# Kernel tuning notes

Hardware: AMD Instinct MI355X
Metric: run time of the kernel (lower is better)

## Reference

```python
import jax, jax.numpy as jnp
import numpy as np

ALPHA = 0.1  # config['alpha']


def setup_inputs() -> dict:
    key = jax.random.key(0)
    k1, k2, k3, k4, k5 = jax.random.split(key, 5)
    n_bs, bit, n_cls, class_bit, n_train = 128, 48, 100, 16, 10000
    u = jax.random.normal(k1, (n_bs, bit), dtype=jnp.float32)
    # multi-hot labels (float, as in torch: y.float())
    y = jax.random.bernoulli(k2, 0.1, (n_bs, n_cls)).astype(jnp.float32)
    ind = jnp.arange(n_bs, dtype=jnp.int64)  # distinct in-range row indices
    # buffers mid-training: U holds previous class-wise codes, Y previous labels
    U = jax.random.normal(k3, (n_train, n_cls, class_bit), dtype=jnp.float32) * 0.1
    Y = jax.random.bernoulli(k4, 0.1, (n_train, n_cls)).astype(jnp.float32)
    # xavier_uniform-like init for w_D [n_class, bit, class_bit]
    limit = np.sqrt(6.0 / (bit + class_bit)).astype(np.float32)
    w_D = jax.random.uniform(k5, (n_cls, bit, class_bit), dtype=jnp.float32,
                             minval=-limit, maxval=limit)
    return {"u": u, "y": y, "ind": ind, "U": U, "Y": Y, "w_D": w_D}


def reference(u, y, ind, U, Y, w_D):
    # update label buffer: self.Y[ind, :] = y
    Y = Y.at[ind].set(y)
    # u_ = matmul(u, w_D).permute(1,0,2): [n_bs, n_cls, class_bit]
    u_ = jnp.einsum('bk,ckd->bcd', u, w_D)
    # update code buffer with detached u_ (torch: self.U[ind] = u_.data)
    U = U.at[ind].set(jax.lax.stop_gradient(u_))
    # pairwise similarity s: [n_bs, n_train, n_cls]
    s = y[:, None, :] * Y[None, :, :]
    # inner_product: sum over class_bit -> [n_bs, n_train, n_cls]
    ip = jnp.einsum('tcd,bcd->btc', U, u_)
    # stable log(1 + exp(ip)) - s*ip, exactly as the torch expression
    likelihood = (jnp.log1p(jnp.exp(-jnp.abs(ip))) + jnp.maximum(ip, 0.0)
                  - s * ip).mean()
    quantization = ALPHA * jnp.mean((u_ - jnp.sign(u_)) ** 2)
    return likelihood + quantization
```

## Files before the change

### kernel.cpp

```cpp
#include <hip/hip_runtime.h>
#include <math.h>

#define CB 16
#define ALPHA 0.1f
#define LOG2E 1.4426950408889634f

typedef __bf16 bf16x8 __attribute__((ext_vector_type(8)));
typedef float  f32x16 __attribute__((ext_vector_type(16)));

__device__ __forceinline__ unsigned int f2bf(float x) {
    unsigned int u = __float_as_uint(x);
    return (u + 0x7FFFu + ((u >> 16) & 1u)) >> 16;
}

__device__ inline float block_reduce_256(float v, float* red) {
    #pragma unroll
    for (int off = 32; off > 0; off >>= 1) v += __shfl_down(v, off, 64);
    int lane = threadIdx.x & 63;
    int wid  = threadIdx.x >> 6;
    if (lane == 0) red[wid] = v;
    __syncthreads();
    float s = 0.f;
    if (threadIdx.x == 0) {
        int nw = blockDim.x >> 6;
        for (int w = 0; w < nw; ++w) s += red[w];
    }
    return s;
}

__global__ __launch_bounds__(256) void compute_u_kernel(
        const float* __restrict__ u, const float* __restrict__ w_D,
        float* __restrict__ u_f32, unsigned short* __restrict__ u_bf,
        float* __restrict__ quant_partials, int* __restrict__ inv,
        int n_bs, int bit, int n_cls, int n_train) {
    __shared__ float red[4];
    int idx = blockIdx.x * blockDim.x + threadIdx.x;
    if (idx < n_train) inv[idx] = -1;
    int total = n_bs * n_cls * CB;
    float q = 0.f;
    if (idx < total) {
        int d = idx & (CB - 1);
        int c = (idx / CB) % n_cls;
        int b = idx / (CB * n_cls);
        const float* __restrict__ ur = u + (size_t)b * bit;
        const float* __restrict__ w  = w_D + (size_t)c * bit * CB + d;
        float s = 0.f;
        for (int k = 0; k < bit; ++k) s = fmaf(ur[k], w[k * CB], s);
        u_f32[idx] = s;
        u_bf[((size_t)c * n_bs + b) * CB + d] = (unsigned short)f2bf(s * LOG2E);
        float sgn = (s > 0.f) ? 1.f : ((s < 0.f) ? -1.f : 0.f);
        float dd = s - sgn;
        q = dd * dd;
    }
    float bs = block_reduce_256(q, red);
    if (threadIdx.x == 0) quant_partials[blockIdx.x] = bs;
}

__global__ __launch_bounds__(256) void compute_vw_kernel(
        const float* __restrict__ y, const float* __restrict__ u_f32,
        const int* __restrict__ ind, int* __restrict__ inv,
        float* __restrict__ vvec, float* __restrict__ wvec,
        int n_bs, int n_cls) {
    if (blockIdx.x == 0 && threadIdx.x < n_bs)
        inv[ind[threadIdx.x]] = threadIdx.x;
    __shared__ float vs[16][17];
    __shared__ float wsh[16][17];
    const int c  = blockIdx.x;
    const int d  = threadIdx.x & (CB - 1);
    const int sl = threadIdx.x >> 4;
    float v = 0.f, w = 0.f;
    const int bpp = n_bs >> 4;
    for (int b = sl * bpp; b < (sl + 1) * bpp; ++b) {
        float x = u_f32[((size_t)b * n_cls + c) * CB + d];
        w += x;
        v = fmaf(y[(size_t)b * n_cls + c], x, v);
    }
    vs[sl][d] = v; wsh[sl][d] = w;
    __syncthreads();
    #pragma unroll
    for (int s = 8; s > 0; s >>= 1) {
        if (sl < s) {
            vs[sl][d]  += vs[sl + s][d];
            wsh[sl][d] += wsh[sl + s][d];
        }
        __syncthreads();
    }
    if (sl == 0) {
        vvec[(size_t)c * CB + d] = vs[0][d];
        wvec[(size_t)c * CB + d] = wsh[0][d];
    }
}

__global__ __launch_bounds__(256) void loss_main_mfma(
        const float* __restrict__ y, const float* __restrict__ U,
        const float* __restrict__ Yb, const float* __restrict__ u_f32,
        const unsigned short* __restrict__ u_bf,
        const float* __restrict__ vvec, const float* __restrict__ wvec,
        const int* __restrict__ inv, float* __restrict__ partials, int nblk,
        int n_bs, int n_cls, int n_train) {
    __shared__ float red[4 * 4];
    const int lane = threadIdx.x & 63;
    const int wid  = threadIdx.x >> 6;
    const int c    = blockIdx.x * 4 + wid;
    const int t0   = blockIdx.y * 32;
    const int r    = lane & 31;
    const int h    = lane >> 5;
    const int row  = t0 + r;

    const bool valid = (row < n_train);
    const int rc = valid ? row : (n_train - 1);
    const int iv = inv[rc];

    const float* __restrict__ arow = (iv >= 0)
        ? (u_f32 + ((size_t)iv * n_cls + c) * CB)
        : (U     + ((size_t)rc * n_cls + c) * CB);
    float4 a0 = *(const float4*)(arow + h * 8);
    float4 a1 = *(const float4*)(arow + h * 8 + 4);
    const float* __restrict__ yrow = (iv >= 0)
        ? (y  + (size_t)iv * n_cls + c)
        : (Yb + (size_t)rc * n_cls + c);
    float Yv = *yrow;
    if (!valid) {
        a0 = make_float4(0.f, 0.f, 0.f, 0.f);
        a1 = make_float4(0.f, 0.f, 0.f, 0.f);
        Yv = 0.f;
    }

    const float* __restrict__ vp = vvec + (size_t)c * CB + h * 8;
    const float* __restrict__ wp = wvec + (size_t)c * CB + h * 8;
    float sv = a0.x*vp[0] + a0.y*vp[1] + a0.z*vp[2] + a0.w*vp[3]
             + a1.x*vp[4] + a1.y*vp[5] + a1.z*vp[6] + a1.w*vp[7];
    float sw = a0.x*wp[0] + a0.y*wp[1] + a0.z*wp[2] + a0.w*wp[3]
             + a1.x*wp[4] + a1.y*wp[5] + a1.z*wp[6] + a1.w*wp[7];
    float sideS = Yv * sv;
    float sideW = sw;

    union { unsigned int u32[4]; bf16x8 v; } A;
    A.u32[0] = f2bf(a0.x) | (f2bf(a0.y) << 16);
    A.u32[1] = f2bf(a0.z) | (f2bf(a0.w) << 16);
    A.u32[2] = f2bf(a1.x) | (f2bf(a1.y) << 16);
    A.u32[3] = f2bf(a1.z) | (f2bf(a1.w) << 16);

    const unsigned short* __restrict__ ub = u_bf + (size_t)c * n_bs * CB;
    bf16x8 B[4];
    #pragma unroll
    for (int bt = 0; bt < 4; ++bt)
        B[bt] = *(const bf16x8*)(ub + (size_t)(bt * 32 + r) * CB + h * 8);

    float accL = 0.f;
    float accA = 0.f;
    f32x16 zc = {};
    #pragma unroll
    for (int bt = 0; bt < 4; ++bt) {
        f32x16 D = __builtin_amdgcn_mfma_f32_32x32x16_bf16(A.v, B[bt], zc, 0, 0, 0);
        float a[16];
        #pragma unroll
        for (int j = 0; j < 16; ++j) {
            float ipa = fabsf(D[j]);
            a[j] = 1.0f + __builtin_amdgcn_exp2f(-ipa);
            accA += ipa;
        }
        #pragma unroll
        for (int s = 1; s < 16; s <<= 1)
            #pragma unroll
            for (int j = 0; j < 16; j += 2 * s) a[j] *= a[j + s];
        accL += __builtin_amdgcn_logf(a[0]);
    }

    #pragma unroll
    for (int off = 32; off > 0; off >>= 1) {
        accL  += __shfl_down(accL,  off, 64);
        accA  += __shfl_down(accA,  off, 64);
        sideS += __shfl_down(sideS, off, 64);
        sideW += __shfl_down(sideW, off, 64);
    }
    if (lane == 0) {
        red[wid * 4 + 0] = accL;
        red[wid * 4 + 1] = accA;
        red[wid * 4 + 2] = sideS;
        red[wid * 4 + 3] = sideW;
    }
    __syncthreads();
    if (threadIdx.x < 4) {
        float s = red[0 * 4 + threadIdx.x] + red[1 * 4 + threadIdx.x]
                + red[2 * 4 + threadIdx.x] + red[3 * 4 + threadIdx.x];
        int bid = blockIdx.y * gridDim.x + blockIdx.x;
        partials[(size_t)threadIdx.x * nblk + bid] = s;
    }
}

__global__ __launch_bounds__(256) void finalize_kernel(
        const float* __restrict__ partials, int nblk,
        const float* __restrict__ quant_partials, int n_quant,
        float* __restrict__ out, double n_pad,
        double like_scale, double quant_scale) {
    double sL = 0, sA = 0, sS = 0, sW = 0, sQ = 0;
    for (int i = threadIdx.x; i < nblk; i += 256) {
        sL += (double)partials[0 * nblk + i];
        sA += (double)partials[1 * nblk + i];
        sS += (double)partials[2 * nblk + i];
        sW += (double)partials[3 * nblk + i];
    }
    for (int i = threadIdx.x; i < n_quant; i += 256) sQ += (double)quant_partials[i];
    #pragma unroll
    for (int off = 32; off > 0; off >>= 1) {
        sL += __shfl_down(sL, off, 64);
        sA += __shfl_down(sA, off, 64);
        sS += __shfl_down(sS, off, 64);
        sW += __shfl_down(sW, off, 64);
        sQ += __shfl_down(sQ, off, 64);
    }
    __shared__ double red[4][5];
    int lane = threadIdx.x & 63, wid = threadIdx.x >> 6;
    if (lane == 0) {
        red[wid][0] = sL; red[wid][1] = sA; red[wid][2] = sS;
        red[wid][3] = sW; red[wid][4] = sQ;
    }
    __syncthreads();
    if (threadIdx.x == 0) {
        double L = 0, Aa = 0, S = 0, W = 0, Q = 0;
        for (int w = 0; w < 4; ++w) {
            L += red[w][0]; Aa += red[w][1]; S += red[w][2];
            W += red[w][3]; Q  += red[w][4];
        }
        const double ln2 = 0.6931471805599453;
        double like = ln2 * (L - n_pad + 0.5 * Aa) + 0.5 * W - S;
        out[0] = (float)(like * like_scale + Q * quant_scale);
    }
}

extern "C" void kernel_launch(void* const* d_in, const int* in_sizes, int n_in,
                              void* d_out, int out_size, void* d_ws, size_t ws_size,
                              hipStream_t stream) {
    const float* u   = (const float*)d_in[0];
    const float* y   = (const float*)d_in[1];
    const int*   ind = (const int*)d_in[2];
    const float* U   = (const float*)d_in[3];
    const float* Yb  = (const float*)d_in[4];
    const float* w_D = (const float*)d_in[5];

    const int n_bs    = in_sizes[2];
    const int bit     = in_sizes[0] / n_bs;
    const int n_cls   = in_sizes[1] / n_bs;
    const int n_train = in_sizes[4] / n_cls;

    const int totalU = n_bs * n_cls * CB;
    const int nub    = (totalU + 255) / 256;
    const int ntile  = (n_train + 31) / 32;
    const int gx     = (n_cls + 3) / 4;
    const int nblk   = ntile * gx;

    char* ws = (char*)d_ws;
    size_t off = 0;
    float* u_f32 = (float*)(ws + off);          off += (size_t)totalU * 4;
    unsigned short* u_bf = (unsigned short*)(ws + off); off += (size_t)totalU * 2;
    off = (off + 15) & ~(size_t)15;
    int* inv = (int*)(ws + off);                off += (size_t)n_train * 4;
    off = (off + 15) & ~(size_t)15;
    float* vvec = (float*)(ws + off);           off += (size_t)n_cls * CB * 4;
    float* wvec = (float*)(ws + off);           off += (size_t)n_cls * CB * 4;
    float* quant_partials = (float*)(ws + off); off += (size_t)nub * 4;
    off = (off + 15) & ~(size_t)15;
    float* partials = (float*)(ws + off);       off += (size_t)nblk * 4 * 4;

    compute_u_kernel<<<nub, 256, 0, stream>>>(u, w_D, u_f32, u_bf,
                                              quant_partials, inv,
                                              n_bs, bit, n_cls, n_train);
    compute_vw_kernel<<<n_cls, 256, 0, stream>>>(y, u_f32, ind, inv,
                                                 vvec, wvec, n_bs, n_cls);
    loss_main_mfma<<<dim3(gx, ntile), 256, 0, stream>>>(
        y, U, Yb, u_f32, u_bf, vvec, wvec, inv, partials, nblk,
        n_bs, n_cls, n_train);

    const double n_pad = (double)((long long)(ntile * 32 - n_train) *
                                  (long long)n_bs * (long long)n_cls);
    const double like_scale  = 1.0 / ((double)n_bs * n_train * n_cls);
    const double quant_scale = (double)ALPHA / (double)totalU;
    finalize_kernel<<<1, 256, 0, stream>>>(partials, nblk, quant_partials, nub,
                                           (float*)d_out, n_pad,
                                           like_scale, quant_scale);
}
```

Measured before the change: 59.79 us.

## Merge prep kernels, drop inverse-index buffer, process two row tiles per wave

Merges the u_ computation and the v/w vector computation into one prep kernel. The v/w vectors are now computed algebraically from sums over u and the weights, so they no longer depend on u_f32 and that pass can run concurrently. The inv scatter buffer is removed; each loss block builds a per-block list of overridden rows from ind in shared memory. Each wave now covers 64 training rows with two A fragments and eight MFMAs, halving the grid and reusing the B loads. This saves one kernel launch and the dependent-launch serialization, at the cost of a per-block scan of ind and a serial patch loop.

```diff
diff --git a/kernel.cpp b/kernel.cpp
--- a/kernel.cpp
+++ b/kernel.cpp
@@ -7,11 +7,6 @@
 
 typedef __bf16 bf16x8 __attribute__((ext_vector_type(8)));
 typedef float  f32x16 __attribute__((ext_vector_type(16)));
-
-__device__ __forceinline__ unsigned int f2bf(float x) {
-    unsigned int u = __float_as_uint(x);
-    return (u + 0x7FFFu + ((u >> 16) & 1u)) >> 16;
-}
 
 __device__ inline float block_reduce_256(float v, float* red) {
     #pragma unroll
@@ -28,120 +23,161 @@
     return s;
 }
 
-__global__ __launch_bounds__(256) void compute_u_kernel(
-        const float* __restrict__ u, const float* __restrict__ w_D,
-        float* __restrict__ u_f32, unsigned short* __restrict__ u_bf,
-        float* __restrict__ quant_partials, int* __restrict__ inv,
-        int n_bs, int bit, int n_cls, int n_train) {
+__global__ __launch_bounds__(256) void prep_kernel(
+        const float* __restrict__ u, const float* __restrict__ y,
+        const float* __restrict__ w_D,
+        float* __restrict__ u_f32, __bf16* __restrict__ u_bf,
+        float* __restrict__ quant_partials,
+        float* __restrict__ vvec, float* __restrict__ wvec,
+        int n_bs, int bit, int n_cls, int nub) {
     __shared__ float red[4];
-    int idx = blockIdx.x * blockDim.x + threadIdx.x;
-    if (idx < n_train) inv[idx] = -1;
-    int total = n_bs * n_cls * CB;
-    float q = 0.f;
-    if (idx < total) {
-        int d = idx & (CB - 1);
-        int c = (idx / CB) % n_cls;
-        int b = idx / (CB * n_cls);
-        const float* __restrict__ ur = u + (size_t)b * bit;
-        const float* __restrict__ w  = w_D + (size_t)c * bit * CB + d;
-        float s = 0.f;
-        for (int k = 0; k < bit; ++k) s = fmaf(ur[k], w[k * CB], s);
-        u_f32[idx] = s;
-        u_bf[((size_t)c * n_bs + b) * CB + d] = (unsigned short)f2bf(s * LOG2E);
-        float sgn = (s > 0.f) ? 1.f : ((s < 0.f) ? -1.f : 0.f);
-        float dd = s - sgn;
-        q = dd * dd;
-    }
-    float bs = block_reduce_256(q, red);
-    if (threadIdx.x == 0) quant_partials[blockIdx.x] = bs;
-}
-
-__global__ __launch_bounds__(256) void compute_vw_kernel(
-        const float* __restrict__ y, const float* __restrict__ u_f32,
-        const int* __restrict__ ind, int* __restrict__ inv,
-        float* __restrict__ vvec, float* __restrict__ wvec,
-        int n_bs, int n_cls) {
-    if (blockIdx.x == 0 && threadIdx.x < n_bs)
-        inv[ind[threadIdx.x]] = threadIdx.x;
-    __shared__ float vs[16][17];
-    __shared__ float wsh[16][17];
-    const int c  = blockIdx.x;
-    const int d  = threadIdx.x & (CB - 1);
-    const int sl = threadIdx.x >> 4;
-    float v = 0.f, w = 0.f;
-    const int bpp = n_bs >> 4;
-    for (int b = sl * bpp; b < (sl + 1) * bpp; ++b) {
-        float x = u_f32[((size_t)b * n_cls + c) * CB + d];
-        w += x;
-        v = fmaf(y[(size_t)b * n_cls + c], x, v);
-    }
-    vs[sl][d] = v; wsh[sl][d] = w;
-    __syncthreads();
-    #pragma unroll
-    for (int s = 8; s > 0; s >>= 1) {
-        if (sl < s) {
-            vs[sl][d]  += vs[sl + s][d];
-            wsh[sl][d] += wsh[sl + s][d];
-        }
+    __shared__ float yus[4][64];
+    __shared__ float sus[4][64];
+    if ((int)blockIdx.x < nub) {
+        int idx = blockIdx.x * 256 + threadIdx.x;
+        int total = n_bs * n_cls * CB;
+        float q = 0.f;
+        if (idx < total) {
+            int d = idx & (CB - 1);
+            int c = (idx / CB) % n_cls;
+            int b = idx / (CB * n_cls);
+            const float* __restrict__ ur = u + (size_t)b * bit;
+            const float* __restrict__ w  = w_D + (size_t)c * bit * CB + d;
+            float s = 0.f;
+            for (int k = 0; k < bit; ++k) s = fmaf(ur[k], w[k * CB], s);
+            u_f32[idx] = s;
+            u_bf[((size_t)c * n_bs + b) * CB + d] = (__bf16)(s * LOG2E);
+            float sgn = (s > 0.f) ? 1.f : ((s < 0.f) ? -1.f : 0.f);
+            float dd = s - sgn;
+            q = dd * dd;
+        }
+        float bs = block_reduce_256(q, red);
+        if (threadIdx.x == 0) quant_partials[blockIdx.x] = bs;
+    } else {
+        const int c  = blockIdx.x - nub;
+        const int kk = threadIdx.x & 63;
+        const int sl = threadIdx.x >> 6;
+        float yv = 0.f, sv = 0.f;
+        if (kk < bit) {
+            const int bpp = n_bs >> 2;
+            for (int b = sl * bpp; b < (sl + 1) * bpp; ++b) {
+                float uv = u[(size_t)b * bit + kk];
+                sv += uv;
+                yv = fmaf(y[(size_t)b * n_cls + c], uv, yv);
+            }
+        }
+        yus[sl][kk] = yv; sus[sl][kk] = sv;
         __syncthreads();
-    }
-    if (sl == 0) {
-        vvec[(size_t)c * CB + d] = vs[0][d];
-        wvec[(size_t)c * CB + d] = wsh[0][d];
+        if (sl == 0 && kk < bit) {
+            yus[0][kk] = yus[0][kk] + yus[1][kk] + yus[2][kk] + yus[3][kk];
+            sus[0][kk] = sus[0][kk] + sus[1][kk] + sus[2][kk] + sus[3][kk];
+        }
+        __syncthreads();
+        if (threadIdx.x < CB) {
+            const int d = threadIdx.x;
+            const float* __restrict__ wdc = w_D + (size_t)c * bit * CB + d;
+            float v = 0.f, w = 0.f;
+            for (int k = 0; k < bit; ++k) {
+                float wv = wdc[k * CB];
+                v = fmaf(yus[0][k], wv, v);
+                w = fmaf(sus[0][k], wv, w);
+            }
+            vvec[(size_t)c * CB + d] = v;
+            wvec[(size_t)c * CB + d] = w;
+        }
     }
 }
 
 __global__ __launch_bounds__(256) void loss_main_mfma(
         const float* __restrict__ y, const float* __restrict__ U,
         const float* __restrict__ Yb, const float* __restrict__ u_f32,
-        const unsigned short* __restrict__ u_bf,
+        const __bf16* __restrict__ u_bf,
         const float* __restrict__ vvec, const float* __restrict__ wvec,
-        const int* __restrict__ inv, float* __restrict__ partials, int nblk,
+        const int* __restrict__ ind, float* __restrict__ partials, int nblk,
         int n_bs, int n_cls, int n_train) {
     __shared__ float red[4 * 4];
-    const int lane = threadIdx.x & 63;
-    const int wid  = threadIdx.x >> 6;
+    __shared__ int plist[64];
+    __shared__ int pn;
+    const int tid  = threadIdx.x;
+    const int lane = tid & 63;
+    const int wid  = tid >> 6;
     const int c    = blockIdx.x * 4 + wid;
-    const int t0   = blockIdx.y * 32;
+    const int t0   = blockIdx.y * 64;
     const int r    = lane & 31;
     const int h    = lane >> 5;
-    const int row  = t0 + r;
-
-    const bool valid = (row < n_train);
-    const int rc = valid ? row : (n_train - 1);
-    const int iv = inv[rc];
-
-    const float* __restrict__ arow = (iv >= 0)
-        ? (u_f32 + ((size_t)iv * n_cls + c) * CB)
-        : (U     + ((size_t)rc * n_cls + c) * CB);
-    float4 a0 = *(const float4*)(arow + h * 8);
-    float4 a1 = *(const float4*)(arow + h * 8 + 4);
-    const float* __restrict__ yrow = (iv >= 0)
-        ? (y  + (size_t)iv * n_cls + c)
-        : (Yb + (size_t)rc * n_cls + c);
-    float Yv = *yrow;
-    if (!valid) {
-        a0 = make_float4(0.f, 0.f, 0.f, 0.f);
-        a1 = make_float4(0.f, 0.f, 0.f, 0.f);
-        Yv = 0.f;
+    const int row0 = t0 + r;
+    const int row1 = t0 + 32 + r;
+
+    if (tid == 0) pn = 0;
+
+    const int rc0 = (row0 < n_train) ? row0 : (n_train - 1);
+    const int rc1 = (row1 < n_train) ? row1 : (n_train - 1);
+    const float* __restrict__ ar0 = U + ((size_t)rc0 * n_cls + c) * CB + h * 8;
+    const float* __restrict__ ar1 = U + ((size_t)rc1 * n_cls + c) * CB + h * 8;
+    float4 a00 = *(const float4*)(ar0);
+    float4 a01 = *(const float4*)(ar0 + 4);
+    float4 a10 = *(const float4*)(ar1);
+    float4 a11 = *(const float4*)(ar1 + 4);
+    float Yv0 = Yb[(size_t)rc0 * n_cls + c];
+    float Yv1 = Yb[(size_t)rc1 * n_cls + c];
+
+    __syncthreads();
+    if (tid < n_bs) {
+        int t = ind[tid];
+        int rl = t - t0;
+        if (rl >= 0 && rl < 64) {
+            int s = atomicAdd(&pn, 1);
+            plist[s] = (rl << 16) | tid;
+        }
+    }
+    __syncthreads();
+
+    const int np = pn;
+    for (int i = 0; i < np; ++i) {
+        int p  = plist[i];
+        int rl = p >> 16;
+        int b  = p & 0xFFFF;
+        if ((rl & 31) == r) {
+            const float* __restrict__ src =
+                u_f32 + ((size_t)b * n_cls + c) * CB + h * 8;
+            float4 p0 = *(const float4*)(src);
+            float4 p1 = *(const float4*)(src + 4);
+            float  py = y[(size_t)b * n_cls + c];
+            if (rl < 32) { a00 = p0; a01 = p1; Yv0 = py; }
+            else         { a10 = p0; a11 = p1; Yv1 = py; }
+        }
+    }
+    if (row0 >= n_train) {
+        a00 = make_float4(0.f,0.f,0.f,0.f); a01 = a00; Yv0 = 0.f;
+    }
+    if (row1 >= n_train) {
+        a10 = make_float4(0.f,0.f,0.f,0.f); a11 = a10; Yv1 = 0.f;
     }
 
     const float* __restrict__ vp = vvec + (size_t)c * CB + h * 8;
     const float* __restrict__ wp = wvec + (size_t)c * CB + h * 8;
-    float sv = a0.x*vp[0] + a0.y*vp[1] + a0.z*vp[2] + a0.w*vp[3]
-             + a1.x*vp[4] + a1.y*vp[5] + a1.z*vp[6] + a1.w*vp[7];
-    float sw = a0.x*wp[0] + a0.y*wp[1] + a0.z*wp[2] + a0.w*wp[3]
-             + a1.x*wp[4] + a1.y*wp[5] + a1.z*wp[6] + a1.w*wp[7];
-    float sideS = Yv * sv;
-    float sideW = sw;
-
-    union { unsigned int u32[4]; bf16x8 v; } A;
-    A.u32[0] = f2bf(a0.x) | (f2bf(a0.y) << 16);
-    A.u32[1] = f2bf(a0.z) | (f2bf(a0.w) << 16);
-    A.u32[2] = f2bf(a1.x) | (f2bf(a1.y) << 16);
-    A.u32[3] = f2bf(a1.z) | (f2bf(a1.w) << 16);
-
-    const unsigned short* __restrict__ ub = u_bf + (size_t)c * n_bs * CB;
+    float sv0 = a00.x*vp[0] + a00.y*vp[1] + a00.z*vp[2] + a00.w*vp[3]
+              + a01.x*vp[4] + a01.y*vp[5] + a01.z*vp[6] + a01.w*vp[7];
+    float sw0 = a00.x*wp[0] + a00.y*wp[1] + a00.z*wp[2] + a00.w*wp[3]
+              + a01.x*wp[4] + a01.y*wp[5] + a01.z*wp[6] + a01.w*wp[7];
+    float sv1 = a10.x*vp[0] + a10.y*vp[1] + a10.z*vp[2] + a10.w*vp[3]
+              + a11.x*vp[4] + a11.y*vp[5] + a11.z*vp[6] + a11.w*vp[7];
+    float sw1 = a10.x*wp[0] + a10.y*wp[1] + a10.z*wp[2] + a10.w*wp[3]
+              + a11.x*wp[4] + a11.y*wp[5] + a11.z*wp[6] + a11.w*wp[7];
+    float sideS = Yv0 * sv0 + Yv1 * sv1;
+    float sideW = sw0 + sw1;
+
+    bf16x8 A[2];
+    A[0][0] = (__bf16)a00.x; A[0][1] = (__bf16)a00.y;
+    A[0][2] = (__bf16)a00.z; A[0][3] = (__bf16)a00.w;
+    A[0][4] = (__bf16)a01.x; A[0][5] = (__bf16)a01.y;
+    A[0][6] = (__bf16)a01.z; A[0][7] = (__bf16)a01.w;
+    A[1][0] = (__bf16)a10.x; A[1][1] = (__bf16)a10.y;
+    A[1][2] = (__bf16)a10.z; A[1][3] = (__bf16)a10.w;
+    A[1][4] = (__bf16)a11.x; A[1][5] = (__bf16)a11.y;
+    A[1][6] = (__bf16)a11.z; A[1][7] = (__bf16)a11.w;
+
+    const __bf16* __restrict__ ub = u_bf + (size_t)c * n_bs * CB;
     bf16x8 B[4];
     #pragma unroll
     for (int bt = 0; bt < 4; ++bt)
@@ -151,20 +187,24 @@
     float accA = 0.f;
     f32x16 zc = {};
     #pragma unroll
-    for (int bt = 0; bt < 4; ++bt) {
-        f32x16 D = __builtin_amdgcn_mfma_f32_32x32x16_bf16(A.v, B[bt], zc, 0, 0, 0);
-        float a[16];
+    for (int at = 0; at < 2; ++at) {
         #pragma unroll
-        for (int j = 0; j < 16; ++j) {
-            float ipa = fabsf(D[j]);
-            a[j] = 1.0f + __builtin_amdgcn_exp2f(-ipa);
-            accA += ipa;
-        }
-        #pragma unroll
-        for (int s = 1; s < 16; s <<= 1)
+        for (int bt = 0; bt < 4; ++bt) {
+            f32x16 D = __builtin_amdgcn_mfma_f32_32x32x16_bf16(
+                           A[at], B[bt], zc, 0, 0, 0);
+            float a[16];
             #pragma unroll
-            for (int j = 0; j < 16; j += 2 * s) a[j] *= a[j + s];
-        accL += __builtin_amdgcn_logf(a[0]);
+            for (int j = 0; j < 16; ++j) {
+                float ipa = fabsf(D[j]);
+                a[j] = 1.0f + __builtin_amdgcn_exp2f(-ipa);
+                accA += ipa;
+            }
+            #pragma unroll
+            for (int s = 1; s < 16; s <<= 1)
+                #pragma unroll
+                for (int j = 0; j < 16; j += 2 * s) a[j] *= a[j + s];
+            accL += __builtin_amdgcn_logf(a[0]);
+        }
     }
 
     #pragma unroll
@@ -181,11 +221,11 @@
         red[wid * 4 + 3] = sideW;
     }
     __syncthreads();
-    if (threadIdx.x < 4) {
-        float s = red[0 * 4 + threadIdx.x] + red[1 * 4 + threadIdx.x]
-                + red[2 * 4 + threadIdx.x] + red[3 * 4 + threadIdx.x];
+    if (tid < 4) {
+        float s = red[0 * 4 + tid] + red[1 * 4 + tid]
+                + red[2 * 4 + tid] + red[3 * 4 + tid];
         int bid = blockIdx.y * gridDim.x + blockIdx.x;
-        partials[(size_t)threadIdx.x * nblk + bid] = s;
+        partials[(size_t)tid * nblk + bid] = s;
     }
 }
 
@@ -246,16 +286,14 @@
 
     const int totalU = n_bs * n_cls * CB;
     const int nub    = (totalU + 255) / 256;
-    const int ntile  = (n_train + 31) / 32;
+    const int ntile  = (n_train + 63) / 64;
     const int gx     = (n_cls + 3) / 4;
     const int nblk   = ntile * gx;
 
     char* ws = (char*)d_ws;
     size_t off = 0;
     float* u_f32 = (float*)(ws + off);          off += (size_t)totalU * 4;
-    unsigned short* u_bf = (unsigned short*)(ws + off); off += (size_t)totalU * 2;
-    off = (off + 15) & ~(size_t)15;
-    int* inv = (int*)(ws + off);                off += (size_t)n_train * 4;
+    __bf16* u_bf = (__bf16*)(ws + off);         off += (size_t)totalU * 2;
     off = (off + 15) & ~(size_t)15;
     float* vvec = (float*)(ws + off);           off += (size_t)n_cls * CB * 4;
     float* wvec = (float*)(ws + off);           off += (size_t)n_cls * CB * 4;
@@ -263,16 +301,14 @@
     off = (off + 15) & ~(size_t)15;
     float* partials = (float*)(ws + off);       off += (size_t)nblk * 4 * 4;
 
-    compute_u_kernel<<<nub, 256, 0, stream>>>(u, w_D, u_f32, u_bf,
-                                              quant_partials, inv,
-                                              n_bs, bit, n_cls, n_train);
-    compute_vw_kernel<<<n_cls, 256, 0, stream>>>(y, u_f32, ind, inv,
-                                                 vvec, wvec, n_bs, n_cls);
+    prep_kernel<<<nub + n_cls, 256, 0, stream>>>(
+        u, y, w_D, u_f32, u_bf, quant_partials, vvec, wvec,
+        n_bs, bit, n_cls, nub);
     loss_main_mfma<<<dim3(gx, ntile), 256, 0, stream>>>(
-        y, U, Yb, u_f32, u_bf, vvec, wvec, inv, partials, nblk,
+        y, U, Yb, u_f32, u_bf, vvec, wvec, ind, partials, nblk,
         n_bs, n_cls, n_train);
 
-    const double n_pad = (double)((long long)(ntile * 32 - n_train) *
+    const double n_pad = (double)((long long)(ntile * 64 - n_train) *
                                   (long long)n_bs * (long long)n_cls);
     const double like_scale  = 1.0 / ((double)n_bs * n_train * n_cls);
     const double quant_scale = (double)ALPHA / (double)totalU;
```

New measurement: 60.92 us. Within noise of the previous version (+1.9%).
